# Kernel optimization log

Hardware: AMD Instinct MI355X
Metric: run time of the kernel (lower is better)

The kernel has to match this reference:

```python
import jax, jax.numpy as jnp
import numpy as np


def setup_inputs() -> dict:
    key = jax.random.key(0)
    embeddings = jax.random.normal(key, (4, 2048, 128), dtype=jnp.float32)
    return {"embeddings": embeddings}


def _pairwise_dist(x):
    # x: [N, D] -> Euclidean distance matrix [N, N] (matches torch.cdist, p=2)
    sq = jnp.sum(x * x, axis=-1)  # [N]
    d2 = sq[:, None] + sq[None, :] - 2.0 * (x @ x.T)
    d2 = jnp.maximum(d2, 0.0)
    # safe sqrt: exact 0 on the diagonal / coincident points, no NaN grads
    safe = jnp.where(d2 > 0.0, d2, 1.0)
    return jnp.where(d2 > 0.0, jnp.sqrt(safe), 0.0)


def reference(embeddings) -> jnp.ndarray:
    b, s, d = embeddings.shape
    x = embeddings.reshape(b * s, d)
    dist = _pairwise_dist(x)                 # [N, N]
    mean_dist = jnp.mean(dist)
    # torch.std default: unbiased (ddof=1) over all elements
    std_dist = jnp.std(dist, ddof=1)
    return std_dist / (mean_dist + 1e-08)
```

## Files before the change

kernel.cpp:

```cpp
#include <hip/hip_runtime.h>
#include <hip/hip_bf16.h>
#include <math.h>


#define NPTS   8192
#define DIM    128
#define BT     256
#define NT2    (NPTS / BT)
#define NBLK   (NT2 * (NT2 + 1) / 2)
#define NTILES (NPTS / 128)
#define NTOTSQ (NTILES * NTILES)

typedef __attribute__((ext_vector_type(8))) short short8;
typedef __attribute__((ext_vector_type(4))) float f32x4;

typedef const __attribute__((address_space(1))) void* gas_ptr;
typedef __attribute__((address_space(3))) void* las_ptr;

__device__ __forceinline__ void gload16(const void* g, void* l) {
    __builtin_amdgcn_global_load_lds((gas_ptr)g, (las_ptr)l, 16, 0, 0);
}

__device__ __forceinline__ float fsqrt(float x) {
    return __builtin_amdgcn_sqrtf(x);
}

__global__ __launch_bounds__(256)
void ph_prep(const float* __restrict__ x, ushort* __restrict__ xb,
             float* __restrict__ sq)
{
    const int tid = threadIdx.x;
    const int row = blockIdx.x * 32 + (tid >> 3);
    const int seg = tid & 7;
    const float4* p = reinterpret_cast<const float4*>(x + (size_t)row * DIM + seg * 16);
    float v[16];
    {
        float4 a = p[0], b = p[1], c = p[2], d = p[3];
        v[0]=a.x; v[1]=a.y; v[2]=a.z; v[3]=a.w;  v[4]=b.x; v[5]=b.y; v[6]=b.z; v[7]=b.w;
        v[8]=c.x; v[9]=c.y; v[10]=c.z; v[11]=c.w; v[12]=d.x; v[13]=d.y; v[14]=d.z; v[15]=d.w;
    }
    float s = 0.f;
    ushort h[16];
#pragma unroll
    for (int j = 0; j < 16; ++j) {
        __hip_bfloat16 hb = __float2bfloat16(v[j]);
        h[j] = *reinterpret_cast<ushort*>(&hb);
        s = fmaf(v[j], v[j], s);
    }
    short8 o0, o1;
#pragma unroll
    for (int j = 0; j < 8; ++j) { o0[j] = (short)h[j]; o1[j] = (short)h[j+8]; }
    short8* dst = reinterpret_cast<short8*>(xb + (size_t)row * DIM + seg * 16);
    dst[0] = o0; dst[1] = o1;
    s += __shfl_xor(s, 1); s += __shfl_xor(s, 2); s += __shfl_xor(s, 4);
    if (seg == 0) sq[row] = s;
}

__global__ __launch_bounds__(512)
void ph_gram(const ushort* __restrict__ xb, const float* __restrict__ sq,
             double* __restrict__ partials)
{
    const int f   = blockIdx.x;
    const int tid = threadIdx.x;

    int bi = (int)((65.0f - fsqrt((float)(4225 - 8 * f))) * 0.5f);
    while ((bi + 1) * 32 - ((bi + 1) * bi) / 2 <= f) ++bi;
    while (bi * 32 - (bi * (bi - 1)) / 2 > f) --bi;
    const int bj = bi + (f - (bi * 32 - (bi * (bi - 1)) / 2));

    __shared__ ushort A0[BT * 64], B0[BT * 64];
    __shared__ ushort A1[BT * 64], B1[BT * 64];
    __shared__ double rr[16];

    const int lane = tid & 63;
    const int wv   = tid >> 6;
    const int wr2  = wv >> 2;
    const int wc4  = wv & 3;

    const char* gA = (const char*)(xb + (size_t)bi * BT * DIM);
    const char* gB = (const char*)(xb + (size_t)bj * BT * DIM);

    const bool  stA  = wv < 4;
    const char* gsrc = stA ? gA : gB;
    const int   cb0  = (wv & 3) * 8;
    const int   srow = lane >> 3;
    const int   skb  = (lane & 7) * 16;

#define STAGE(h, dA, dB)                                                      \
    {                                                                         \
        char* dst_ = stA ? (char*)(dA) : (char*)(dB);                         \
        _Pragma("unroll")                                                     \
        for (int c = 0; c < 8; ++c) {                                         \
            const int chunk = cb0 + c;                                        \
            const int row   = chunk * 8 + srow;                               \
            const size_t go = (size_t)row * 256 + (h) * 128                   \
                              + (skb ^ ((row & 7) << 4));                     \
            gload16(gsrc + go, dst_ + chunk * 1024);                          \
        }                                                                     \
    }

    f32x4 acc[8][4];
#pragma unroll
    for (int m = 0; m < 8; ++m)
#pragma unroll
        for (int n = 0; n < 4; ++n) acc[m][n] = (f32x4){0.f, 0.f, 0.f, 0.f};

#define COMPUTE(dA, dB)                                                       \
    {                                                                         \
        _Pragma("unroll")                                                     \
        for (int ks = 0; ks < 2; ++ks) {                                      \
            const int kb = ks * 64 + (lane >> 4) * 16;                        \
            short8 af[8], bfr[4];                                             \
            _Pragma("unroll")                                                 \
            for (int m = 0; m < 8; ++m) {                                     \
                const int row = wr2 * 128 + m * 16 + (lane & 15);             \
                af[m] = *reinterpret_cast<const short8*>(                     \
                    (const char*)(dA) + row * 128 + (kb ^ ((row & 7) << 4))); \
            }                                                                 \
            _Pragma("unroll")                                                 \
            for (int n = 0; n < 4; ++n) {                                     \
                const int col = wc4 * 64 + n * 16 + (lane & 15);              \
                bfr[n] = *reinterpret_cast<const short8*>(                    \
                    (const char*)(dB) + col * 128 + (kb ^ ((col & 7) << 4))); \
            }                                                                 \
            _Pragma("unroll")                                                 \
            for (int m = 0; m < 8; ++m)                                       \
                _Pragma("unroll")                                             \
                for (int n = 0; n < 4; ++n)                                   \
                    acc[m][n] = __builtin_amdgcn_mfma_f32_16x16x32_bf16(      \
                        af[m], bfr[n], acc[m][n], 0, 0, 0);                   \
        }                                                                     \
    }

    STAGE(0, A0, B0);
    __syncthreads();
    STAGE(1, A1, B1);
    COMPUTE(A0, B0);
    __syncthreads();
    COMPUTE(A1, B1);

    const float* sqA = sq + bi * BT + wr2 * 128 + (lane >> 4) * 4;
    const float* sqB = sq + bj * BT + wc4 * 64 + (lane & 15);
    float nB_[4];
#pragma unroll
    for (int n = 0; n < 4; ++n) nB_[n] = sqB[n * 16];

    float s1a = 0.f, s1b = 0.f, s2a = 0.f, s2b = 0.f;
    const bool diag = (bi == bj);
    if (!diag) {
#pragma unroll
        for (int m = 0; m < 8; ++m) {
            const float4 na = *reinterpret_cast<const float4*>(sqA + m * 16);
#pragma unroll
            for (int n = 0; n < 4; ++n) {
                float d0 = fmaxf(fmaf(-2.f, acc[m][n][0], na.x + nB_[n]), 0.f);
                float d1 = fmaxf(fmaf(-2.f, acc[m][n][1], na.y + nB_[n]), 0.f);
                float d2 = fmaxf(fmaf(-2.f, acc[m][n][2], na.z + nB_[n]), 0.f);
                float d3 = fmaxf(fmaf(-2.f, acc[m][n][3], na.w + nB_[n]), 0.f);
                s1a += fsqrt(d0); s1b += fsqrt(d1);
                s1a += fsqrt(d2); s1b += fsqrt(d3);
                s2a += d0 + d2;   s2b += d1 + d3;
            }
        }
    } else {
#pragma unroll
        for (int m = 0; m < 8; ++m) {
            const float4 na = *reinterpret_cast<const float4*>(sqA + m * 16);
            const float nav[4] = {na.x, na.y, na.z, na.w};
#pragma unroll
            for (int n = 0; n < 4; ++n) {
                const int col = wc4 * 64 + n * 16 + (lane & 15);
#pragma unroll
                for (int r = 0; r < 4; ++r) {
                    const int row = wr2 * 128 + m * 16 + (lane >> 4) * 4 + r;
                    float d = fmaxf(fmaf(-2.f, acc[m][n][r], nav[r] + nB_[n]), 0.f);
                    if (row == col) d = 0.f;
                    s1a += fsqrt(d);
                    s2a += d;
                }
            }
        }
    }
    float s1 = s1a + s1b, s2 = s2a + s2b;
#pragma unroll
    for (int off = 1; off < 64; off <<= 1) {
        s1 += __shfl_xor(s1, off);
        s2 += __shfl_xor(s2, off);
    }
    const double w = diag ? 1.0 : 2.0;
    if (lane == 0) { rr[wv] = (double)s1 * w; rr[8 + wv] = (double)s2 * w; }
    __syncthreads();
    if (tid == 0) {
        double t1 = 0.0, t2 = 0.0;
#pragma unroll
        for (int i = 0; i < 8; ++i) { t1 += rr[i]; t2 += rr[8 + i]; }
        partials[2*f] = t1; partials[2*f + 1] = t2;
    }
#undef STAGE
#undef COMPUTE
}

__global__ __launch_bounds__(256)
void ph_finalize(const double* __restrict__ partials, float* __restrict__ out)
{
    __shared__ double r1[256], r2[256];
    const int tid = threadIdx.x;
    double s1 = 0.0, s2 = 0.0;
    for (int i = tid; i < NBLK; i += 256) { s1 += partials[2*i]; s2 += partials[2*i+1]; }
    r1[tid] = s1; r2[tid] = s2;
    __syncthreads();
    for (int off = 128; off > 0; off >>= 1) {
        if (tid < off) { r1[tid] += r1[tid+off]; r2[tid] += r2[tid+off]; }
        __syncthreads();
    }
    if (tid == 0) {
        const double M    = (double)NPTS * (double)NPTS;
        const double mean = r1[0] / M;
        double var = (r2[0] - r1[0]*r1[0]/M) / (M - 1.0);
        if (var < 0.0) var = 0.0;
        out[0] = (float)(sqrt(var) / (mean + 1e-8));
    }
}

#define LSTR 132
__global__ __launch_bounds__(256)
void ph_pair_kernel(const float* __restrict__ x, double* __restrict__ partials)
{
    const int bi  = blockIdx.y;
    const int bj  = blockIdx.x;
    const int tid = threadIdx.x;
    const int flat = bi * NTILES + bj;
    if (bj < bi) {
        if (tid == 0) { partials[2*flat] = 0.0; partials[2*flat+1] = 0.0; }
        return;
    }
    __shared__ __align__(16) float As[128 * LSTR];
    __shared__ __align__(16) float Bs[128 * LSTR];
    __shared__ float  nA[128];
    __shared__ float  nB[128];
    __shared__ double red1[256];
    __shared__ double red2[256];
    const float* Ab = x + (size_t)bi * 128 * DIM;
    const float* Bb = x + (size_t)bj * 128 * DIM;
#pragma unroll
    for (int it = 0; it < 16; ++it) {
        const int e   = (tid + it * 256) * 4;
        const int row = e >> 7;
        const int k   = e & 127;
        float4 va = *reinterpret_cast<const float4*>(Ab + e);
        As[(k+0)*LSTR + row] = va.x; As[(k+1)*LSTR + row] = va.y;
        As[(k+2)*LSTR + row] = va.z; As[(k+3)*LSTR + row] = va.w;
        float4 vb = *reinterpret_cast<const float4*>(Bb + e);
        Bs[(k+0)*LSTR + row] = vb.x; Bs[(k+1)*LSTR + row] = vb.y;
        Bs[(k+2)*LSTR + row] = vb.z; Bs[(k+3)*LSTR + row] = vb.w;
    }
    __syncthreads();
    if (tid < 128) {
        float s = 0.f;
#pragma unroll 8
        for (int k = 0; k < DIM; ++k) { float v = As[k*LSTR + tid]; s = fmaf(v, v, s); }
        nA[tid] = s;
    } else {
        const int r = tid - 128;
        float s = 0.f;
#pragma unroll 8
        for (int k = 0; k < DIM; ++k) { float v = Bs[k*LSTR + r]; s = fmaf(v, v, s); }
        nB[r] = s;
    }
    __syncthreads();
    const int tx = tid & 15, ty = tid >> 4;
    const int ra = ty * 8, cb = tx * 8;
    float acc[8][8];
#pragma unroll
    for (int r = 0; r < 8; ++r)
#pragma unroll
        for (int c = 0; c < 8; ++c) acc[r][c] = 0.f;
#pragma unroll 4
    for (int k = 0; k < DIM; ++k) {
        const float4 a0 = *reinterpret_cast<const float4*>(&As[k*LSTR + ra]);
        const float4 a1 = *reinterpret_cast<const float4*>(&As[k*LSTR + ra + 4]);
        const float4 b0 = *reinterpret_cast<const float4*>(&Bs[k*LSTR + cb]);
        const float4 b1 = *reinterpret_cast<const float4*>(&Bs[k*LSTR + cb + 4]);
        const float a[8] = {a0.x,a0.y,a0.z,a0.w,a1.x,a1.y,a1.z,a1.w};
        const float b[8] = {b0.x,b0.y,b0.z,b0.w,b1.x,b1.y,b1.z,b1.w};
#pragma unroll
        for (int r = 0; r < 8; ++r)
#pragma unroll
            for (int c = 0; c < 8; ++c)
                acc[r][c] = fmaf(a[r], b[c], acc[r][c]);
    }
    double s1 = 0.0, s2 = 0.0;
    const int gi0 = bi*128 + ra, gj0 = bj*128 + cb;
#pragma unroll
    for (int r = 0; r < 8; ++r) {
#pragma unroll
        for (int c = 0; c < 8; ++c) {
            float d2 = nA[ra+r] + nB[cb+c] - 2.0f * acc[r][c];
            d2 = fmaxf(d2, 0.0f);
            if (gi0 + r == gj0 + c) d2 = 0.0f;
            s1 += (double)sqrtf(d2);
            s2 += (double)d2;
        }
    }
    const double w = (bi == bj) ? 1.0 : 2.0;
    s1 *= w; s2 *= w;
    red1[tid] = s1; red2[tid] = s2;
    __syncthreads();
    for (int off = 128; off > 0; off >>= 1) {
        if (tid < off) { red1[tid] += red1[tid+off]; red2[tid] += red2[tid+off]; }
        __syncthreads();
    }
    if (tid == 0) { partials[2*flat] = red1[0]; partials[2*flat+1] = red2[0]; }
}

__global__ __launch_bounds__(256)
void ph_finalize_sq(const double* __restrict__ partials, float* __restrict__ out)
{
    __shared__ double r1[256], r2[256];
    const int tid = threadIdx.x;
    double s1 = 0.0, s2 = 0.0;
    for (int i = tid; i < NTOTSQ; i += 256) { s1 += partials[2*i]; s2 += partials[2*i+1]; }
    r1[tid] = s1; r2[tid] = s2;
    __syncthreads();
    for (int off = 128; off > 0; off >>= 1) {
        if (tid < off) { r1[tid] += r1[tid+off]; r2[tid] += r2[tid+off]; }
        __syncthreads();
    }
    if (tid == 0) {
        const double M    = (double)NPTS * (double)NPTS;
        const double mean = r1[0] / M;
        double var = (r2[0] - r1[0]*r1[0]/M) / (M - 1.0);
        if (var < 0.0) var = 0.0;
        out[0] = (float)(sqrt(var) / (mean + 1e-8));
    }
}

extern "C" void kernel_launch(void* const* d_in, const int* in_sizes, int n_in,
                              void* d_out, int out_size, void* d_ws, size_t ws_size,
                              hipStream_t stream)
{
    const float* x = (const float*)d_in[0];
    float* out     = (float*)d_out;

    const size_t XB_OFF = 0;
    const size_t SQ_OFF = (size_t)NPTS * DIM * sizeof(ushort);
    const size_t PT_OFF = SQ_OFF + NPTS * sizeof(float);
    const size_t NEEDED = PT_OFF + (size_t)NTOTSQ * 2 * sizeof(double);

    if (ws_size >= NEEDED) {
        ushort* xb       = (ushort*)((char*)d_ws + XB_OFF);
        float*  sq       = (float*) ((char*)d_ws + SQ_OFF);
        double* partials = (double*)((char*)d_ws + PT_OFF);

        ph_prep<<<NPTS / 32, 256, 0, stream>>>(x, xb, sq);
        ph_gram<<<NBLK, 512, 0, stream>>>(xb, sq, partials);
        ph_finalize<<<1, 256, 0, stream>>>(partials, out);
    } else {
        double* partials = (double*)d_ws;
        ph_pair_kernel<<<dim3(NTILES, NTILES), 256, 0, stream>>>(x, partials);
        ph_finalize_sq<<<1, 256, 0, stream>>>(partials, out);
    }
}
```

Measured before the change: 33.75 us.

## Compute squared-distance sum in closed form and pipeline gram K-loop in quarters

The sum of squared distances is now computed analytically as 2N·Σ|x|² − 2|Σx|², using per-block column sums produced in the prep kernel, so the gram epilogue only accumulates square roots. The gram kernel splits K into four 32-wide LDS stages issued with explicit vmcnt waits and raw barriers, and raises wave priority around the MFMA block so loads overlap compute. The LDS XOR swizzle is removed, which may bring bank conflicts. The closed form may lose precision through cancellation, though the final reduction is done in double.

```diff
diff --git a/kernel.cpp b/kernel.cpp
--- a/kernel.cpp
+++ b/kernel.cpp
@@ -8,6 +8,7 @@
 #define BT     256
 #define NT2    (NPTS / BT)
 #define NBLK   (NT2 * (NT2 + 1) / 2)
+#define NPREP  (NPTS / 32)
 #define NTILES (NPTS / 128)
 #define NTOTSQ (NTILES * NTILES)
 
@@ -20,17 +21,21 @@
 __device__ __forceinline__ void gload16(const void* g, void* l) {
     __builtin_amdgcn_global_load_lds((gas_ptr)g, (las_ptr)l, 16, 0, 0);
 }
-
 __device__ __forceinline__ float fsqrt(float x) {
     return __builtin_amdgcn_sqrtf(x);
 }
 
+#define VMCNT(n) asm volatile("s_waitcnt vmcnt(" #n ")" ::: "memory")
+#define RBAR()   __builtin_amdgcn_s_barrier()
+
 __global__ __launch_bounds__(256)
 void ph_prep(const float* __restrict__ x, ushort* __restrict__ xb,
-             float* __restrict__ sq)
-{
+             float* __restrict__ sq, float* __restrict__ cs_part)
+{
+    __shared__ float xs[32][129];
     const int tid = threadIdx.x;
-    const int row = blockIdx.x * 32 + (tid >> 3);
+    const int rw  = tid >> 3;
+    const int row = blockIdx.x * 32 + rw;
     const int seg = tid & 7;
     const float4* p = reinterpret_cast<const float4*>(x + (size_t)row * DIM + seg * 16);
     float v[16];
@@ -46,6 +51,7 @@
         __hip_bfloat16 hb = __float2bfloat16(v[j]);
         h[j] = *reinterpret_cast<ushort*>(&hb);
         s = fmaf(v[j], v[j], s);
+        xs[rw][seg * 16 + j] = v[j];
     }
     short8 o0, o1;
 #pragma unroll
@@ -54,6 +60,13 @@
     dst[0] = o0; dst[1] = o1;
     s += __shfl_xor(s, 1); s += __shfl_xor(s, 2); s += __shfl_xor(s, 4);
     if (seg == 0) sq[row] = s;
+    __syncthreads();
+    if (tid < DIM) {
+        float c = 0.f;
+#pragma unroll 8
+        for (int r = 0; r < 32; ++r) c += xs[r][tid];
+        cs_part[blockIdx.x * DIM + tid] = c;
+    }
 }
 
 __global__ __launch_bounds__(512)
@@ -68,9 +81,9 @@
     while (bi * 32 - (bi * (bi - 1)) / 2 > f) --bi;
     const int bj = bi + (f - (bi * 32 - (bi * (bi - 1)) / 2));
 
-    __shared__ ushort A0[BT * 64], B0[BT * 64];
-    __shared__ ushort A1[BT * 64], B1[BT * 64];
-    __shared__ double rr[16];
+    __shared__ ushort Aq[4][BT * 32];
+    __shared__ ushort Bq[4][BT * 32];
+    __shared__ double rr[8];
 
     const int lane = tid & 63;
     const int wv   = tid >> 6;
@@ -82,19 +95,18 @@
 
     const bool  stA  = wv < 4;
     const char* gsrc = stA ? gA : gB;
-    const int   cb0  = (wv & 3) * 8;
-    const int   srow = lane >> 3;
-    const int   skb  = (lane & 7) * 16;
-
-#define STAGE(h, dA, dB)                                                      \
+    const int   c0   = (wv & 3) * 4;
+    const int   lrow = lane >> 2;
+    const int   lks  = (lane & 3) * 16;
+
+#define STAGE(q)                                                              \
     {                                                                         \
-        char* dst_ = stA ? (char*)(dA) : (char*)(dB);                         \
+        char* dst_ = stA ? (char*)Aq[q] : (char*)Bq[q];                       \
         _Pragma("unroll")                                                     \
-        for (int c = 0; c < 8; ++c) {                                         \
-            const int chunk = cb0 + c;                                        \
-            const int row   = chunk * 8 + srow;                               \
-            const size_t go = (size_t)row * 256 + (h) * 128                   \
-                              + (skb ^ ((row & 7) << 4));                     \
+        for (int c = 0; c < 4; ++c) {                                         \
+            const int chunk = c0 + c;                                         \
+            const int row   = chunk * 16 + lrow;                              \
+            const size_t go = (size_t)row * 256 + (q) * 64 + lks;             \
             gload16(gsrc + go, dst_ + chunk * 1024);                          \
         }                                                                     \
     }
@@ -105,118 +117,152 @@
 #pragma unroll
         for (int n = 0; n < 4; ++n) acc[m][n] = (f32x4){0.f, 0.f, 0.f, 0.f};
 
-#define COMPUTE(dA, dB)                                                       \
+#define COMPUTE(q)                                                            \
     {                                                                         \
+        const int kb = (lane >> 4) * 16;                                      \
+        short8 af[8], bfr[4];                                                 \
         _Pragma("unroll")                                                     \
-        for (int ks = 0; ks < 2; ++ks) {                                      \
-            const int kb = ks * 64 + (lane >> 4) * 16;                        \
-            short8 af[8], bfr[4];                                             \
+        for (int m = 0; m < 8; ++m) {                                         \
+            const int row = wr2 * 128 + m * 16 + (lane & 15);                 \
+            af[m] = *reinterpret_cast<const short8*>(                         \
+                (const char*)Aq[q] + row * 64 + kb);                          \
+        }                                                                     \
+        _Pragma("unroll")                                                     \
+        for (int n = 0; n < 4; ++n) {                                         \
+            const int col = wc4 * 64 + n * 16 + (lane & 15);                  \
+            bfr[n] = *reinterpret_cast<const short8*>(                        \
+                (const char*)Bq[q] + col * 64 + kb);                          \
+        }                                                                     \
+        __builtin_amdgcn_s_setprio(1);                                        \
+        _Pragma("unroll")                                                     \
+        for (int m = 0; m < 8; ++m)                                           \
             _Pragma("unroll")                                                 \
-            for (int m = 0; m < 8; ++m) {                                     \
-                const int row = wr2 * 128 + m * 16 + (lane & 15);             \
-                af[m] = *reinterpret_cast<const short8*>(                     \
-                    (const char*)(dA) + row * 128 + (kb ^ ((row & 7) << 4))); \
-            }                                                                 \
-            _Pragma("unroll")                                                 \
-            for (int n = 0; n < 4; ++n) {                                     \
-                const int col = wc4 * 64 + n * 16 + (lane & 15);              \
-                bfr[n] = *reinterpret_cast<const short8*>(                    \
-                    (const char*)(dB) + col * 128 + (kb ^ ((col & 7) << 4))); \
-            }                                                                 \
-            _Pragma("unroll")                                                 \
-            for (int m = 0; m < 8; ++m)                                       \
-                _Pragma("unroll")                                             \
-                for (int n = 0; n < 4; ++n)                                   \
-                    acc[m][n] = __builtin_amdgcn_mfma_f32_16x16x32_bf16(      \
-                        af[m], bfr[n], acc[m][n], 0, 0, 0);                   \
-        }                                                                     \
-    }
-
-    STAGE(0, A0, B0);
-    __syncthreads();
-    STAGE(1, A1, B1);
-    COMPUTE(A0, B0);
-    __syncthreads();
-    COMPUTE(A1, B1);
+            for (int n = 0; n < 4; ++n)                                       \
+                acc[m][n] = __builtin_amdgcn_mfma_f32_16x16x32_bf16(          \
+                    af[m], bfr[n], acc[m][n], 0, 0, 0);                       \
+        __builtin_amdgcn_s_setprio(0);                                        \
+    }
+
+    STAGE(0);
+    STAGE(1);
+    VMCNT(4); RBAR();
+    COMPUTE(0);
+    STAGE(2);
+    VMCNT(4); RBAR();
+    COMPUTE(1);
+    STAGE(3);
 
     const float* sqA = sq + bi * BT + wr2 * 128 + (lane >> 4) * 4;
     const float* sqB = sq + bj * BT + wc4 * 64 + (lane & 15);
-    float nB_[4];
-#pragma unroll
-    for (int n = 0; n < 4; ++n) nB_[n] = sqB[n * 16];
-
-    float s1a = 0.f, s1b = 0.f, s2a = 0.f, s2b = 0.f;
+    float4 na[4];
+    float  nb[4];
+#pragma unroll
+    for (int m = 0; m < 4; ++m) na[m] = *reinterpret_cast<const float4*>(sqA + m * 32);
+#pragma unroll
+    for (int n = 0; n < 4; ++n) nb[n] = sqB[n * 16];
+
+    VMCNT(12); RBAR();
+    COMPUTE(2);
+    VMCNT(8); RBAR();
+    COMPUTE(3);
+    VMCNT(0);
+
+    float s1a = 0.f, s1b = 0.f, s1c = 0.f, s1d = 0.f;
     const bool diag = (bi == bj);
     if (!diag) {
 #pragma unroll
-        for (int m = 0; m < 8; ++m) {
-            const float4 na = *reinterpret_cast<const float4*>(sqA + m * 16);
+        for (int m = 0; m < 4; ++m) {
+            const float4 v = na[m];
 #pragma unroll
             for (int n = 0; n < 4; ++n) {
-                float d0 = fmaxf(fmaf(-2.f, acc[m][n][0], na.x + nB_[n]), 0.f);
-                float d1 = fmaxf(fmaf(-2.f, acc[m][n][1], na.y + nB_[n]), 0.f);
-                float d2 = fmaxf(fmaf(-2.f, acc[m][n][2], na.z + nB_[n]), 0.f);
-                float d3 = fmaxf(fmaf(-2.f, acc[m][n][3], na.w + nB_[n]), 0.f);
-                s1a += fsqrt(d0); s1b += fsqrt(d1);
-                s1a += fsqrt(d2); s1b += fsqrt(d3);
-                s2a += d0 + d2;   s2b += d1 + d3;
+                s1a += fsqrt(fmaxf(fmaf(-2.f, acc[2*m][n][0], v.x + nb[n]), 0.f));
+                s1b += fsqrt(fmaxf(fmaf(-2.f, acc[2*m][n][1], v.y + nb[n]), 0.f));
+                s1c += fsqrt(fmaxf(fmaf(-2.f, acc[2*m][n][2], v.z + nb[n]), 0.f));
+                s1d += fsqrt(fmaxf(fmaf(-2.f, acc[2*m][n][3], v.w + nb[n]), 0.f));
+            }
+        }
+    }
+    if (!diag) {
+#pragma unroll
+        for (int m = 1; m < 8; m += 2) {
+            const float4 v = *reinterpret_cast<const float4*>(sqA + m * 16);
+#pragma unroll
+            for (int n = 0; n < 4; ++n) {
+                s1a += fsqrt(fmaxf(fmaf(-2.f, acc[m][n][0], v.x + nb[n]), 0.f));
+                s1b += fsqrt(fmaxf(fmaf(-2.f, acc[m][n][1], v.y + nb[n]), 0.f));
+                s1c += fsqrt(fmaxf(fmaf(-2.f, acc[m][n][2], v.z + nb[n]), 0.f));
+                s1d += fsqrt(fmaxf(fmaf(-2.f, acc[m][n][3], v.w + nb[n]), 0.f));
             }
         }
     } else {
 #pragma unroll
         for (int m = 0; m < 8; ++m) {
-            const float4 na = *reinterpret_cast<const float4*>(sqA + m * 16);
-            const float nav[4] = {na.x, na.y, na.z, na.w};
+            const float4 v = *reinterpret_cast<const float4*>(sqA + m * 16);
+            const float nav[4] = {v.x, v.y, v.z, v.w};
 #pragma unroll
             for (int n = 0; n < 4; ++n) {
                 const int col = wc4 * 64 + n * 16 + (lane & 15);
 #pragma unroll
                 for (int r = 0; r < 4; ++r) {
                     const int row = wr2 * 128 + m * 16 + (lane >> 4) * 4 + r;
-                    float d = fmaxf(fmaf(-2.f, acc[m][n][r], nav[r] + nB_[n]), 0.f);
+                    float d = fmaxf(fmaf(-2.f, acc[m][n][r], nav[r] + nb[n]), 0.f);
                     if (row == col) d = 0.f;
                     s1a += fsqrt(d);
-                    s2a += d;
                 }
             }
         }
     }
-    float s1 = s1a + s1b, s2 = s2a + s2b;
-#pragma unroll
-    for (int off = 1; off < 64; off <<= 1) {
-        s1 += __shfl_xor(s1, off);
-        s2 += __shfl_xor(s2, off);
-    }
+    float s1 = (s1a + s1b) + (s1c + s1d);
+#pragma unroll
+    for (int off = 1; off < 64; off <<= 1) s1 += __shfl_xor(s1, off);
     const double w = diag ? 1.0 : 2.0;
-    if (lane == 0) { rr[wv] = (double)s1 * w; rr[8 + wv] = (double)s2 * w; }
+    if (lane == 0) rr[wv] = (double)s1 * w;
     __syncthreads();
     if (tid == 0) {
-        double t1 = 0.0, t2 = 0.0;
-#pragma unroll
-        for (int i = 0; i < 8; ++i) { t1 += rr[i]; t2 += rr[8 + i]; }
-        partials[2*f] = t1; partials[2*f + 1] = t2;
+        double t1 = 0.0;
+#pragma unroll
+        for (int i = 0; i < 8; ++i) t1 += rr[i];
+        partials[f] = t1;
     }
 #undef STAGE
 #undef COMPUTE
 }
 
 __global__ __launch_bounds__(256)
-void ph_finalize(const double* __restrict__ partials, float* __restrict__ out)
-{
-    __shared__ double r1[256], r2[256];
+void ph_finalize(const double* __restrict__ partials, const float* __restrict__ sq,
+                 const float* __restrict__ cs_part, float* __restrict__ out)
+{
+    __shared__ double r1[256], r2[256], r3[128];
     const int tid = threadIdx.x;
-    double s1 = 0.0, s2 = 0.0;
-    for (int i = tid; i < NBLK; i += 256) { s1 += partials[2*i]; s2 += partials[2*i+1]; }
-    r1[tid] = s1; r2[tid] = s2;
+    double s1 = 0.0;
+    for (int i = tid; i < NBLK; i += 256) s1 += partials[i];
+    double sn = 0.0;
+    for (int k = 0; k < NPTS / 256; ++k) sn += (double)sq[tid + k * 256];
+    r1[tid] = s1; r2[tid] = sn;
+    if (tid < DIM) {
+        double c = 0.0;
+        for (int b = 0; b < NPREP; ++b) c += (double)cs_part[b * DIM + tid];
+        r3[tid] = c * c;
+    }
     __syncthreads();
     for (int off = 128; off > 0; off >>= 1) {
-        if (tid < off) { r1[tid] += r1[tid+off]; r2[tid] += r2[tid+off]; }
+        if (tid < off) {
+            r1[tid] += r1[tid + off];
+            r2[tid] += r2[tid + off];
+            if (off >= 2 && tid < (off >> 1) && off <= 128) {}
+        }
+        __syncthreads();
+    }
+    for (int off = 64; off > 0; off >>= 1) {
+        if (tid < off) r3[tid] += r3[tid + off];
         __syncthreads();
     }
     if (tid == 0) {
         const double M    = (double)NPTS * (double)NPTS;
-        const double mean = r1[0] / M;
-        double var = (r2[0] - r1[0]*r1[0]/M) / (M - 1.0);
+        const double S1   = r1[0];
+        const double S2   = 2.0 * (double)NPTS * r2[0] - 2.0 * r3[0];
+        const double mean = S1 / M;
+        double var = (S2 - S1 * S1 / M) / (M - 1.0);
         if (var < 0.0) var = 0.0;
         out[0] = (float)(sqrt(var) / (mean + 1e-8));
     }
@@ -344,17 +390,19 @@
 
     const size_t XB_OFF = 0;
     const size_t SQ_OFF = (size_t)NPTS * DIM * sizeof(ushort);
-    const size_t PT_OFF = SQ_OFF + NPTS * sizeof(float);
-    const size_t NEEDED = PT_OFF + (size_t)NTOTSQ * 2 * sizeof(double);
+    const size_t CS_OFF = SQ_OFF + NPTS * sizeof(float);
+    const size_t PT_OFF = CS_OFF + (size_t)NPREP * DIM * sizeof(float);
+    const size_t NEEDED = PT_OFF + (size_t)NBLK * sizeof(double);
 
     if (ws_size >= NEEDED) {
         ushort* xb       = (ushort*)((char*)d_ws + XB_OFF);
         float*  sq       = (float*) ((char*)d_ws + SQ_OFF);
+        float*  cs_part  = (float*) ((char*)d_ws + CS_OFF);
         double* partials = (double*)((char*)d_ws + PT_OFF);
 
-        ph_prep<<<NPTS / 32, 256, 0, stream>>>(x, xb, sq);
+        ph_prep<<<NPREP, 256, 0, stream>>>(x, xb, sq, cs_part);
         ph_gram<<<NBLK, 512, 0, stream>>>(xb, sq, partials);
-        ph_finalize<<<1, 256, 0, stream>>>(partials, out);
+        ph_finalize<<<1, 256, 0, stream>>>(partials, sq, cs_part, out);
     } else {
         double* partials = (double*)d_ws;
         ph_pair_kernel<<<dim3(NTILES, NTILES), 256, 0, stream>>>(x, partials);
```

New measurement: 39.72 us. 1.18x slower.

## Make gram kernel persistent over 256 blocks with A-tile reuse across pairs

Applied to the files above, without the earlier changes.

Instead of one block per upper-triangular 256x256 tile pair (528 blocks), launches 256 blocks that each process 2-3 consecutive pairs. A row tile is kept in LDS and reused while the column tile is restaged with double buffering, so the launch count matches the CU count and wave tails shrink. Partial sums accumulate in float across pairs, and finalize now reads exactly 256 partials. The cost is more serial work per block, sync points inside the loop, and slightly less precise float accumulation.

```diff
diff --git a/kernel.cpp b/kernel.cpp
--- a/kernel.cpp
+++ b/kernel.cpp
@@ -7,7 +7,9 @@
 #define DIM    128
 #define BT     256
 #define NT2    (NPTS / BT)
-#define NBLK   (NT2 * (NT2 + 1) / 2)
+#define NPAIR  (NT2 * (NT2 + 1) / 2)
+#define NGBLK  256
+#define NPREP  (NPTS / 32)
 #define NTILES (NPTS / 128)
 #define NTOTSQ (NTILES * NTILES)
 
@@ -20,7 +22,6 @@
 __device__ __forceinline__ void gload16(const void* g, void* l) {
     __builtin_amdgcn_global_load_lds((gas_ptr)g, (las_ptr)l, 16, 0, 0);
 }
-
 __device__ __forceinline__ float fsqrt(float x) {
     return __builtin_amdgcn_sqrtf(x);
 }
@@ -60,16 +61,19 @@
 void ph_gram(const ushort* __restrict__ xb, const float* __restrict__ sq,
              double* __restrict__ partials)
 {
-    const int f   = blockIdx.x;
+    const int b   = blockIdx.x;
     const int tid = threadIdx.x;
 
-    int bi = (int)((65.0f - fsqrt((float)(4225 - 8 * f))) * 0.5f);
-    while ((bi + 1) * 32 - ((bi + 1) * bi) / 2 <= f) ++bi;
-    while (bi * 32 - (bi * (bi - 1)) / 2 > f) --bi;
-    const int bj = bi + (f - (bi * 32 - (bi * (bi - 1)) / 2));
-
-    __shared__ ushort A0[BT * 64], B0[BT * 64];
-    __shared__ ushort A1[BT * 64], B1[BT * 64];
+    const int pstart = (b < 16) ? 3 * b : 48 + 2 * (b - 16);
+    const int pcnt   = (b < 16) ? 3 : 2;
+
+    int si = (int)((65.0f - fsqrt((float)(4225 - 8 * pstart))) * 0.5f);
+    while ((si + 1) * 32 - ((si + 1) * si) / 2 <= pstart) ++si;
+    while (si * 32 - (si * (si - 1)) / 2 > pstart) --si;
+    int tj = si + (pstart - (si * 32 - (si * (si - 1)) / 2));
+
+    __shared__ ushort A0[BT * 64], A1[BT * 64];
+    __shared__ ushort B0[BT * 64], B1[BT * 64];
     __shared__ double rr[16];
 
     const int lane = tid & 63;
@@ -77,34 +81,40 @@
     const int wr2  = wv >> 2;
     const int wc4  = wv & 3;
 
-    const char* gA = (const char*)(xb + (size_t)bi * BT * DIM);
-    const char* gB = (const char*)(xb + (size_t)bj * BT * DIM);
-
-    const bool  stA  = wv < 4;
-    const char* gsrc = stA ? gA : gB;
-    const int   cb0  = (wv & 3) * 8;
-    const int   srow = lane >> 3;
-    const int   skb  = (lane & 7) * 16;
-
-#define STAGE(h, dA, dB)                                                      \
+    const int srow = lane >> 3;
+    const int skb  = (lane & 7) * 16;
+
+    const char* gAp = (const char*)(xb + (size_t)si * BT * DIM);
+    const char* gBp = (const char*)(xb + (size_t)tj * BT * DIM);
+
+#define STAGE_A()                                                             \
     {                                                                         \
-        char* dst_ = stA ? (char*)(dA) : (char*)(dB);                         \
+        const int h_ = wv >> 2;                                               \
+        char* dst_ = h_ ? (char*)A1 : (char*)A0;                              \
         _Pragma("unroll")                                                     \
         for (int c = 0; c < 8; ++c) {                                         \
-            const int chunk = cb0 + c;                                        \
+            const int chunk = (wv & 3) * 8 + c;                               \
+            const int row   = chunk * 8 + srow;                               \
+            const size_t go = (size_t)row * 256 + h_ * 128                    \
+                              + (skb ^ ((row & 7) << 4));                     \
+            gload16(gAp + go, dst_ + chunk * 1024);                           \
+        }                                                                     \
+    }
+
+#define STAGE_B(h, buf)                                                       \
+    {                                                                         \
+        char* dst_ = (char*)(buf);                                            \
+        _Pragma("unroll")                                                     \
+        for (int c = 0; c < 4; ++c) {                                         \
+            const int chunk = wv * 4 + c;                                     \
             const int row   = chunk * 8 + srow;                               \
             const size_t go = (size_t)row * 256 + (h) * 128                   \
                               + (skb ^ ((row & 7) << 4));                     \
-            gload16(gsrc + go, dst_ + chunk * 1024);                          \
+            gload16(gBp + go, dst_ + chunk * 1024);                           \
         }                                                                     \
     }
 
     f32x4 acc[8][4];
-#pragma unroll
-    for (int m = 0; m < 8; ++m)
-#pragma unroll
-        for (int n = 0; n < 4; ++n) acc[m][n] = (f32x4){0.f, 0.f, 0.f, 0.f};
-
 #define COMPUTE(dA, dB)                                                       \
     {                                                                         \
         _Pragma("unroll")                                                     \
@@ -132,71 +142,105 @@
         }                                                                     \
     }
 
-    STAGE(0, A0, B0);
-    __syncthreads();
-    STAGE(1, A1, B1);
-    COMPUTE(A0, B0);
-    __syncthreads();
-    COMPUTE(A1, B1);
-
-    const float* sqA = sq + bi * BT + wr2 * 128 + (lane >> 4) * 4;
-    const float* sqB = sq + bj * BT + wc4 * 64 + (lane & 15);
-    float nB_[4];
-#pragma unroll
-    for (int n = 0; n < 4; ++n) nB_[n] = sqB[n * 16];
-
-    float s1a = 0.f, s1b = 0.f, s2a = 0.f, s2b = 0.f;
-    const bool diag = (bi == bj);
-    if (!diag) {
-#pragma unroll
-        for (int m = 0; m < 8; ++m) {
-            const float4 na = *reinterpret_cast<const float4*>(sqA + m * 16);
-#pragma unroll
-            for (int n = 0; n < 4; ++n) {
-                float d0 = fmaxf(fmaf(-2.f, acc[m][n][0], na.x + nB_[n]), 0.f);
-                float d1 = fmaxf(fmaf(-2.f, acc[m][n][1], na.y + nB_[n]), 0.f);
-                float d2 = fmaxf(fmaf(-2.f, acc[m][n][2], na.z + nB_[n]), 0.f);
-                float d3 = fmaxf(fmaf(-2.f, acc[m][n][3], na.w + nB_[n]), 0.f);
-                s1a += fsqrt(d0); s1b += fsqrt(d1);
-                s1a += fsqrt(d2); s1b += fsqrt(d3);
-                s2a += d0 + d2;   s2b += d1 + d3;
-            }
+    STAGE_A();
+    STAGE_B(0, B0);
+
+    int   csi = si, ctj = tj;
+    float s1t = 0.f, s2t = 0.f;
+
+    for (int it = 0; it < pcnt; ++it) {
+        __syncthreads();
+
+        STAGE_B(1, B1);
+#pragma unroll
+        for (int m = 0; m < 8; ++m)
+#pragma unroll
+            for (int n = 0; n < 4; ++n) acc[m][n] = (f32x4){0.f, 0.f, 0.f, 0.f};
+        COMPUTE(A0, B0);
+
+        int nsi = csi, ntj = ctj + 1;
+        if (ntj == NT2) { ++nsi; ntj = nsi; }
+        const bool more  = (it + 1 < pcnt);
+        const bool cross = more && (nsi != csi);
+
+        __syncthreads();
+        if (more && !cross) {
+            gBp = (const char*)(xb + (size_t)ntj * BT * DIM);
+            STAGE_B(0, B0);
         }
-    } else {
-#pragma unroll
-        for (int m = 0; m < 8; ++m) {
-            const float4 na = *reinterpret_cast<const float4*>(sqA + m * 16);
-            const float nav[4] = {na.x, na.y, na.z, na.w};
-#pragma unroll
-            for (int n = 0; n < 4; ++n) {
-                const int col = wc4 * 64 + n * 16 + (lane & 15);
-#pragma unroll
-                for (int r = 0; r < 4; ++r) {
-                    const int row = wr2 * 128 + m * 16 + (lane >> 4) * 4 + r;
-                    float d = fmaxf(fmaf(-2.f, acc[m][n][r], nav[r] + nB_[n]), 0.f);
-                    if (row == col) d = 0.f;
-                    s1a += fsqrt(d);
-                    s2a += d;
+        COMPUTE(A1, B1);
+
+        const float* sqA = sq + csi * BT + wr2 * 128 + (lane >> 4) * 4;
+        const float* sqB = sq + ctj * BT + wc4 * 64 + (lane & 15);
+        float nb[4];
+#pragma unroll
+        for (int n = 0; n < 4; ++n) nb[n] = sqB[n * 16];
+
+        float s1a = 0.f, s1b = 0.f, s2a = 0.f, s2b = 0.f;
+        const bool diag = (csi == ctj);
+        if (!diag) {
+#pragma unroll
+            for (int m = 0; m < 8; ++m) {
+                const float4 v = *reinterpret_cast<const float4*>(sqA + m * 16);
+#pragma unroll
+                for (int n = 0; n < 4; ++n) {
+                    float d0 = fmaxf(fmaf(-2.f, acc[m][n][0], v.x + nb[n]), 0.f);
+                    float d1 = fmaxf(fmaf(-2.f, acc[m][n][1], v.y + nb[n]), 0.f);
+                    float d2 = fmaxf(fmaf(-2.f, acc[m][n][2], v.z + nb[n]), 0.f);
+                    float d3 = fmaxf(fmaf(-2.f, acc[m][n][3], v.w + nb[n]), 0.f);
+                    s1a += fsqrt(d0); s1b += fsqrt(d1);
+                    s1a += fsqrt(d2); s1b += fsqrt(d3);
+                    s2a += d0 + d2;   s2b += d1 + d3;
                 }
             }
+            s1t += 2.f * ((s1a + s1b));
+            s2t += 2.f * ((s2a + s2b));
+        } else {
+#pragma unroll
+            for (int m = 0; m < 8; ++m) {
+                const float4 v = *reinterpret_cast<const float4*>(sqA + m * 16);
+                const float nav[4] = {v.x, v.y, v.z, v.w};
+#pragma unroll
+                for (int n = 0; n < 4; ++n) {
+                    const int col = wc4 * 64 + n * 16 + (lane & 15);
+#pragma unroll
+                    for (int r = 0; r < 4; ++r) {
+                        const int row = wr2 * 128 + m * 16 + (lane >> 4) * 4 + r;
+                        float d = fmaxf(fmaf(-2.f, acc[m][n][r], nav[r] + nb[n]), 0.f);
+                        if (row == col) d = 0.f;
+                        s1a += fsqrt(d);
+                        s2a += d;
+                    }
+                }
+            }
+            s1t += s1a; s2t += s2a;
         }
-    }
-    float s1 = s1a + s1b, s2 = s2a + s2b;
+
+        if (cross) {
+            __syncthreads();
+            gAp = (const char*)(xb + (size_t)nsi * BT * DIM);
+            gBp = (const char*)(xb + (size_t)ntj * BT * DIM);
+            STAGE_A();
+            STAGE_B(0, B0);
+        }
+        csi = nsi; ctj = ntj;
+    }
+
 #pragma unroll
     for (int off = 1; off < 64; off <<= 1) {
-        s1 += __shfl_xor(s1, off);
-        s2 += __shfl_xor(s2, off);
-    }
-    const double w = diag ? 1.0 : 2.0;
-    if (lane == 0) { rr[wv] = (double)s1 * w; rr[8 + wv] = (double)s2 * w; }
+        s1t += __shfl_xor(s1t, off);
+        s2t += __shfl_xor(s2t, off);
+    }
+    if (lane == 0) { rr[wv] = (double)s1t; rr[8 + wv] = (double)s2t; }
     __syncthreads();
     if (tid == 0) {
         double t1 = 0.0, t2 = 0.0;
 #pragma unroll
         for (int i = 0; i < 8; ++i) { t1 += rr[i]; t2 += rr[8 + i]; }
-        partials[2*f] = t1; partials[2*f + 1] = t2;
-    }
-#undef STAGE
+        partials[2 * b] = t1; partials[2 * b + 1] = t2;
+    }
+#undef STAGE_A
+#undef STAGE_B
 #undef COMPUTE
 }
 
@@ -205,18 +249,18 @@
 {
     __shared__ double r1[256], r2[256];
     const int tid = threadIdx.x;
-    double s1 = 0.0, s2 = 0.0;
-    for (int i = tid; i < NBLK; i += 256) { s1 += partials[2*i]; s2 += partials[2*i+1]; }
+    double s1 = partials[2 * tid];
+    double s2 = partials[2 * tid + 1];
     r1[tid] = s1; r2[tid] = s2;
     __syncthreads();
     for (int off = 128; off > 0; off >>= 1) {
-        if (tid < off) { r1[tid] += r1[tid+off]; r2[tid] += r2[tid+off]; }
+        if (tid < off) { r1[tid] += r1[tid + off]; r2[tid] += r2[tid + off]; }
         __syncthreads();
     }
     if (tid == 0) {
         const double M    = (double)NPTS * (double)NPTS;
         const double mean = r1[0] / M;
-        double var = (r2[0] - r1[0]*r1[0]/M) / (M - 1.0);
+        double var = (r2[0] - r1[0] * r1[0] / M) / (M - 1.0);
         if (var < 0.0) var = 0.0;
         out[0] = (float)(sqrt(var) / (mean + 1e-8));
     }
@@ -345,15 +389,15 @@
     const size_t XB_OFF = 0;
     const size_t SQ_OFF = (size_t)NPTS * DIM * sizeof(ushort);
     const size_t PT_OFF = SQ_OFF + NPTS * sizeof(float);
-    const size_t NEEDED = PT_OFF + (size_t)NTOTSQ * 2 * sizeof(double);
+    const size_t NEEDED = PT_OFF + (size_t)NGBLK * 2 * sizeof(double);
 
     if (ws_size >= NEEDED) {
         ushort* xb       = (ushort*)((char*)d_ws + XB_OFF);
         float*  sq       = (float*) ((char*)d_ws + SQ_OFF);
         double* partials = (double*)((char*)d_ws + PT_OFF);
 
-        ph_prep<<<NPTS / 32, 256, 0, stream>>>(x, xb, sq);
-        ph_gram<<<NBLK, 512, 0, stream>>>(xb, sq, partials);
+        ph_prep<<<NPREP, 256, 0, stream>>>(x, xb, sq);
+        ph_gram<<<NGBLK, 512, 0, stream>>>(xb, sq, partials);
         ph_finalize<<<1, 256, 0, stream>>>(partials, out);
     } else {
         double* partials = (double*)d_ws;
```

New measurement: 37.06 us. 1.1x slower.
